# Kernel tuning notes

Hardware: AMD Instinct MI355X
Metric: run time of the kernel (lower is better)

The kernel has to match this reference:

```python
import jax, jax.numpy as jnp
from jax import lax
import numpy as np

THRESHOLD = 0.9
KHALF = 5  # conv_kernel_size; full conv width = 2*KHALF + 1 = 11


def _cif_scan(eouts, alpha_norm, elens, ylens, Lp1):
    """Vectorized-over-batch integrate-and-fire scan over time (lax.scan)."""
    B, T, D = eouts.shape
    bidx = jnp.arange(B)
    dt = eouts.dtype

    def step(carry, xs):
        alpha_accum, state, n_tok, fired = carry
        a_t, e_t, t = xs  # a_t: [B], e_t: [B,D], t: scalar int
        alpha_accum = alpha_accum + a_t
        active = (t <= elens - 1) & (n_tok < ylens)
        fire = active & (alpha_accum >= THRESHOLD)
        ak1 = 1.0 - alpha_accum
        ak2 = a_t - ak1
        # attention-weight column for time t
        aw_col = jnp.zeros((B, Lp1), dt)
        w_old = jnp.where(fire, ak1, jnp.where(active, a_t, jnp.zeros((), dt)))
        aw_col = aw_col.at[bidx, n_tok].add(w_old)
        n_new = n_tok + fire.astype(n_tok.dtype)
        aw_col = aw_col.at[bidx, n_new].add(jnp.where(fire, ak2, jnp.zeros((), dt)))
        # fired output row (set once per token slot)
        fire_val = state + ak1[:, None] * e_t
        cur = fired[bidx, n_tok]
        fired = fired.at[bidx, n_tok].set(jnp.where(fire[:, None], fire_val, cur))
        # integrate / reset state
        state = jnp.where(fire[:, None], ak2[:, None] * e_t,
                          jnp.where(active[:, None], state + a_t[:, None] * e_t, state))
        alpha_accum = jnp.where(fire, ak2, alpha_accum)
        return (alpha_accum, state, n_new, fired), aw_col

    init = (jnp.zeros((B,), dt), jnp.zeros((B, D), dt),
            jnp.zeros((B,), jnp.int32), jnp.zeros((B, Lp1, D), dt))
    xs = (jnp.swapaxes(alpha_norm, 0, 1), jnp.swapaxes(eouts, 0, 1),
          jnp.arange(T))
    (_, _, _, fired), aw_cols = lax.scan(step, init, xs)
    aws = jnp.transpose(aw_cols, (1, 2, 0))[:, None]  # [B,1,Lp1,T]
    return fired, aws


def _forward(eouts, conv_w, conv_b, proj_w, proj_b, elens, ylens, L):
    # Conv1d over time, 'same' padding: [B,T,D] -> [B,T,C]
    conv_feat = lax.conv_general_dilated(
        eouts, conv_w, window_strides=(1,), padding=[(KHALF, KHALF)],
        dimension_numbers=('NWC', 'WIO', 'NWC')) + conv_b
    alpha = jax.nn.sigmoid(conv_feat @ proj_w + proj_b)[:, :, 0]  # [B,T]
    alpha_norm = alpha / jnp.sum(alpha, axis=1, keepdims=True) \
        * ylens[:, None].astype(alpha.dtype)
    fired, aws = _cif_scan(eouts, alpha_norm, elens, ylens, L + 1)
    return fired[:, :L], alpha, aws


def setup_inputs():
    key = jax.random.key(0)
    k1, k2, k3, k4, k5 = jax.random.split(key, 5)
    B, T, D, C = 16, 2048, 512, 512
    eouts = jax.random.normal(k1, (B, T, D), jnp.float32)
    elens = jnp.maximum(jax.random.randint(k2, (B,), 0, T), T // 2).astype(jnp.int32)
    ylens = jnp.maximum(jax.random.randint(k3, (B,), 0, 128), 32).astype(jnp.int32)
    conv_w = jax.random.normal(k4, (2 * KHALF + 1, D, C), jnp.float32) * 0.02
    conv_b = jnp.zeros((C,), jnp.float32)
    proj_w = jax.random.normal(k5, (C, 1), jnp.float32) * 0.05
    proj_b = jnp.zeros((1,), jnp.float32)
    return dict(eouts=eouts, conv_w=conv_w, conv_b=conv_b,
                proj_w=proj_w, proj_b=proj_b, elens=elens, ylens=ylens)


def reference(eouts, conv_w, conv_b, proj_w, proj_b, elens, ylens):
    L = int(jnp.max(ylens))  # max_len = ylens.max(), as in the original
    return _forward(eouts, conv_w, conv_b, proj_w, proj_b, elens, ylens, L)
```

## Files before the change

kernel.cpp:

```cpp
#include <hip/hip_runtime.h>
#include <math.h>

#define KHALF 5
#define MAXF 256

__global__ void k_weff(const float* __restrict__ conv_w, const float* __restrict__ conv_b,
                       const float* __restrict__ proj_w, const float* __restrict__ proj_b,
                       float* __restrict__ w_eff, float* __restrict__ b_eff,
                       int KD, int C) {
    int gid = blockIdx.x * blockDim.x + threadIdx.x;
    int wave = gid >> 6;
    int lane = gid & 63;
    if (wave > KD) return;
    float s = 0.f;
    if (wave < KD) {
        const float* row = conv_w + (size_t)wave * C;
        for (int c = lane * 4; c < C; c += 256) {
            float4 v = *reinterpret_cast<const float4*>(row + c);
            float4 w = *reinterpret_cast<const float4*>(proj_w + c);
            s += v.x * w.x + v.y * w.y + v.z * w.z + v.w * w.w;
        }
    } else {
        for (int c = lane; c < C; c += 64) s += conv_b[c] * proj_w[c];
    }
#pragma unroll
    for (int off = 32; off > 0; off >>= 1) s += __shfl_down(s, off, 64);
    if (lane == 0) {
        if (wave < KD) w_eff[wave] = s;
        else           b_eff[0] = s + proj_b[0];
    }
}

__global__ __launch_bounds__(256) void k_qdot(const float* __restrict__ eouts,
                                              const float* __restrict__ w_eff,
                                              float* __restrict__ q, int BT) {
    __shared__ float tile[64 * 68];
    __shared__ float wls[11 * 68];
    __shared__ float part[64 * 89];
    const int u0 = blockIdx.x * 64;
    const int rp = threadIdx.x & 31;
    const int s8 = threadIdx.x >> 5;
    float acc0[11], acc1[11];
#pragma unroll
    for (int k = 0; k < 11; ++k) { acc0[k] = 0.f; acc1[k] = 0.f; }
    for (int c = 0; c < 8; ++c) {
        __syncthreads();
#pragma unroll
        for (int it = 0; it < 4; ++it) {
            int idx = it * 256 + threadIdx.x;
            int r = idx >> 4, j4 = idx & 15;
            float4 v = *reinterpret_cast<const float4*>(
                eouts + (size_t)(u0 + r) * 512 + c * 64 + j4 * 4);
            *reinterpret_cast<float4*>(&tile[r * 68 + j4 * 4]) = v;
        }
        if (threadIdx.x < 176) {
            int k = threadIdx.x >> 4, sl = threadIdx.x & 15;
            float4 wv = *reinterpret_cast<const float4*>(
                w_eff + k * 512 + c * 64 + sl * 4);
            *reinterpret_cast<float4*>(&wls[k * 68 + sl * 4]) = wv;
        }
        __syncthreads();
#pragma unroll
        for (int j4 = 0; j4 < 2; ++j4) {
            const int dl = s8 * 8 + j4 * 4;
            float4 a0 = *reinterpret_cast<const float4*>(&tile[rp * 68 + dl]);
            float4 a1 = *reinterpret_cast<const float4*>(&tile[(rp + 32) * 68 + dl]);
#pragma unroll
            for (int k = 0; k < 11; ++k) {
                float4 wv = *reinterpret_cast<const float4*>(&wls[k * 68 + dl]);
                acc0[k] += a0.x * wv.x + a0.y * wv.y + a0.z * wv.z + a0.w * wv.w;
                acc1[k] += a1.x * wv.x + a1.y * wv.y + a1.z * wv.z + a1.w * wv.w;
            }
        }
    }
    __syncthreads();
#pragma unroll
    for (int k = 0; k < 11; ++k) {
        part[rp * 89 + s8 * 11 + k] = acc0[k];
        part[(rp + 32) * 89 + s8 * 11 + k] = acc1[k];
    }
    __syncthreads();
    if (threadIdx.x < 64) {
        int r = threadIdx.x;
        const float* p = &part[r * 89];
        float o[12];
#pragma unroll
        for (int k = 0; k < 11; ++k) {
            float s0 = (p[0 * 11 + k] + p[1 * 11 + k]) + (p[2 * 11 + k] + p[3 * 11 + k]);
            float s1 = (p[4 * 11 + k] + p[5 * 11 + k]) + (p[6 * 11 + k] + p[7 * 11 + k]);
            o[k] = s0 + s1;
        }
        o[11] = 0.f;
        float4* dst = reinterpret_cast<float4*>(q + (size_t)(u0 + r) * 12);
        dst[0] = make_float4(o[0], o[1], o[2], o[3]);
        dst[1] = make_float4(o[4], o[5], o[6], o[7]);
        dst[2] = make_float4(o[8], o[9], o[10], o[11]);
    }
}

__global__ __launch_bounds__(256) void k_sigpart(const float* __restrict__ q,
                                                 const float* __restrict__ b_eff,
                                                 float* __restrict__ alpha,
                                                 float* __restrict__ partials,
                                                 int T, int tcb) {
    __shared__ float qs[266 * 12];
    __shared__ float psm[4];
    int bx = blockIdx.x;
    int b = bx / tcb, tc = bx % tcb;
    int t0 = tc * 256;
    const float* qb = q + (size_t)b * T * 12;
    const int base = (t0 - 5) * 12;
    const int lim = T * 12;
    for (int i = threadIdx.x; i < 266 * 12; i += 256) {
        int gi = base + i;
        qs[i] = (gi >= 0 && gi < lim) ? qb[gi] : 0.f;
    }
    __syncthreads();
    int t = t0 + threadIdx.x;
    float sacc = b_eff[0];
#pragma unroll
    for (int k = 0; k < 11; ++k) sacc += qs[(threadIdx.x + k) * 12 + k];
    float al = 1.f / (1.f + expf(-sacc));
    alpha[(size_t)b * T + t] = al;
    float s = al;
    int lane = threadIdx.x & 63;
    int w = threadIdx.x >> 6;
#pragma unroll
    for (int off = 32; off > 0; off >>= 1) s += __shfl_down(s, off, 64);
    if (lane == 0) psm[w] = s;
    __syncthreads();
    if (threadIdx.x == 0) {
        float tot = 0.f;
        for (int i = 0; i < 4; ++i) tot += psm[i];
        partials[bx] = tot;
    }
}

__global__ void k_alpha(const float* __restrict__ eouts,
                        const float* __restrict__ w_eff,
                        const float* __restrict__ b_eff,
                        float* __restrict__ alpha,
                        int B, int T, int D) {
    const int W = 2 * KHALF + 1;
    int gid = blockIdx.x * blockDim.x + threadIdx.x;
    int wave = gid >> 6;
    int lane = gid & 63;
    if (wave >= B * T) return;
    int b = wave / T;
    int t = wave - b * T;
    int WD = W * D;
    int t0 = t - KHALF;
    float s = 0.f;
    if (t0 >= 0 && t0 + W <= T) {
        const float* base = eouts + ((size_t)b * T + t0) * D;
        for (int j = lane * 4; j < WD; j += 256) {
            float4 v = *reinterpret_cast<const float4*>(base + j);
            float4 w = *reinterpret_cast<const float4*>(w_eff + j);
            s += v.x * w.x + v.y * w.y + v.z * w.z + v.w * w.w;
        }
    } else {
        const float* base = eouts + (size_t)b * T * D;
        for (int j = lane; j < WD; j += 64) {
            int tt = t0 + j / D;
            if (tt >= 0 && tt < T) {
                int d = j - (j / D) * D;
                s += base[(size_t)tt * D + d] * w_eff[j];
            }
        }
    }
#pragma unroll
    for (int off = 32; off > 0; off >>= 1) s += __shfl_down(s, off, 64);
    if (lane == 0) {
        float logit = s + b_eff[0];
        alpha[(size_t)b * T + t] = 1.f / (1.f + expf(-logit));
    }
}

__global__ void k_chain(const float* __restrict__ alpha_in,
                        int use_part,
                        const float* __restrict__ partials, int npart,
                        const int* __restrict__ elens,
                        const int* __restrict__ ylens,
                        float* __restrict__ alpha_sum,
                        float* __restrict__ anorm,
                        int* __restrict__ n_fired,
                        int* __restrict__ fire_t,
                        float* __restrict__ fire_a1,
                        float* __restrict__ fire_a2,
                        int T, int Lp1) {
    extern __shared__ float an[];
    __shared__ float sm[16];
    __shared__ float stot;
    int b = blockIdx.x;
    const float* row = alpha_in + (size_t)b * T;
    for (int i = threadIdx.x; i < T; i += blockDim.x) an[i] = row[i];
    __syncthreads();
    if (use_part) {
        if (threadIdx.x == 0) {
            float tot = 0.f;
            for (int i = 0; i < npart; ++i) tot += partials[b * npart + i];
            stot = tot;
            alpha_sum[b] = tot;
        }
    } else {
        float s = 0.f;
        for (int i = threadIdx.x; i < T; i += blockDim.x) s += an[i];
        int lane0 = threadIdx.x & 63;
        int w0 = threadIdx.x >> 6;
#pragma unroll
        for (int off = 32; off > 0; off >>= 1) s += __shfl_down(s, off, 64);
        if (lane0 == 0) sm[w0] = s;
        __syncthreads();
        if (threadIdx.x == 0) {
            float tot = 0.f;
            int nw = blockDim.x >> 6;
            for (int i = 0; i < nw; ++i) tot += sm[i];
            stot = tot;
            alpha_sum[b] = tot;
        }
    }
    __syncthreads();
    float ssum = stot;
    float yl = (float)ylens[b];
    float* __restrict__ anb = anorm + (size_t)b * T;
    for (int i = threadIdx.x; i < T; i += blockDim.x) {
        float v = an[i] / ssum * yl;
        an[i] = v;
        anb[i] = v;
    }
    __syncthreads();
    if (threadIdx.x >= 64) return;
    int lane = threadIdx.x;
    int elen = elens[b];
    if (elen > T) elen = T;
    const int ylen = ylens[b];
    int* __restrict__ ft = fire_t + (size_t)b * Lp1;
    float* __restrict__ fa1 = fire_a1 + (size_t)b * Lp1;
    float* __restrict__ fa2 = fire_a2 + (size_t)b * Lp1;
    float accum = 0.f;
    int n = 0;
    bool done = false;
    for (int t0 = 0; t0 < elen && !done; t0 += 64) {
        int nv = elen - t0;
        if (nv > 64) nv = 64;
        float a = (lane < nv) ? an[t0 + lane] : 0.f;
        float P = a;
#pragma unroll
        for (int off = 1; off < 64; off <<= 1) {
            float tmp = __shfl_up(P, off, 64);
            if (lane >= off) P += tmp;
        }
        unsigned long long validmask = (nv == 64) ? ~0ull : ((1ull << nv) - 1ull);
        float base = accum;
        int start = 0;
        while (true) {
            bool cond = (base + P >= 0.9f);
            unsigned long long bal = __ballot(cond) & validmask;
            if (start > 0) bal &= (~0ull) << start;
            if (bal == 0) break;
            int u = __builtin_ctzll(bal);
            float Pu = __shfl(P, u, 64);
            float au = __shfl(a, u, 64);
            float accum_f = base + Pu;
            float ak1 = 1.f - accum_f;
            float ak2 = au - ak1;
            if (lane == 0) { ft[n] = t0 + u; fa1[n] = ak1; fa2[n] = ak2; }
            ++n;
            if (n >= ylen) { done = true; break; }
            base = ak2 - Pu;
            start = u + 1;
            if (start >= nv) break;
        }
        if (!done) {
            float Plast = __shfl(P, nv - 1, 64);
            accum = base + Plast;
        }
    }
    if (lane == 0) n_fired[b] = n;
}

__global__ void k_awfired(const float* __restrict__ eouts,
                          const float* __restrict__ anorm,
                          const int* __restrict__ elens,
                          const int* __restrict__ ylens,
                          const int* __restrict__ n_fired,
                          const int* __restrict__ fire_t,
                          const float* __restrict__ fire_a1,
                          const float* __restrict__ fire_a2,
                          float* __restrict__ aws,
                          float* __restrict__ fired,
                          int T, int D, int L, int Lp1,
                          int AB, int tcpb, int DB) {
    if ((int)blockIdx.x < AB) {
        __shared__ int fts[MAXF];
        __shared__ float a1s[MAXF];
        __shared__ float a2s[MAXF];
        int b = blockIdx.x / tcpb;
        int tc = blockIdx.x % tcpb;
        int nf = n_fired[b];
        for (int i = threadIdx.x; i < nf; i += blockDim.x) {
            fts[i] = fire_t[(size_t)b * Lp1 + i];
            a1s[i] = fire_a1[(size_t)b * Lp1 + i];
            a2s[i] = fire_a2[(size_t)b * Lp1 + i];
        }
        __syncthreads();
        int t = tc * 256 + threadIdx.x;
        if (t >= T) return;
        int elen = elens[b];
        if (elen > T) elen = T;
        int ylen = ylens[b];
        bool active = (t < elen);
        int rowi = 0;
        bool isfire = false;
        float v1 = 0.f, v2 = 0.f;
        if (active) {
            int lo = 0, hi = nf;
            while (lo < hi) {
                int mid = (lo + hi) >> 1;
                if (fts[mid] < t) lo = mid + 1; else hi = mid;
            }
            rowi = lo;
            isfire = (rowi < nf && fts[rowi] == t);
            if (isfire) { v1 = a1s[rowi]; v2 = a2s[rowi]; }
            else if (rowi < ylen) v1 = anorm[(size_t)b * T + t];
            else active = false;
        }
        float* col = aws + (size_t)b * Lp1 * T + t;
        for (int r = 0; r < Lp1; ++r) {
            float v = 0.f;
            if (active) {
                if (r == rowi) v = v1;
                else if (isfire && r == rowi + 1) v = v2;
            }
            col[(size_t)r * T] = v;
        }
    } else {
        int idx = blockIdx.x - AB;
        int b = idx / (L * DB);
        int rem = idx % (L * DB);
        int n = rem / DB;
        int d = (rem % DB) * 256 + threadIdx.x;
        if (d >= D) return;
        int nf = n_fired[b];
        float* dst = fired + ((size_t)b * L + n) * D + d;
        if (n >= nf) { *dst = 0.f; return; }
        int t0 = (n == 0) ? 0 : fire_t[(size_t)b * Lp1 + n - 1];
        int t1 = fire_t[(size_t)b * Lp1 + n];
        float ak1 = fire_a1[(size_t)b * Lp1 + n];
        float ak2p = (n > 0) ? fire_a2[(size_t)b * Lp1 + n - 1] : 0.f;
        const float* an_g = anorm + (size_t)b * T;
        const float* e = eouts + ((size_t)b * T + t0) * D + d;
        float accv = 0.f;
        for (int t = t0; t <= t1; ++t, e += D) {
            float wgt;
            if (t == t1) wgt = ak1;
            else if (t == t0 && n > 0) wgt = ak2p;
            else wgt = an_g[t];
            accv += wgt * e[0];
        }
        *dst = accv;
    }
}

extern "C" void kernel_launch(void* const* d_in, const int* in_sizes, int n_in,
                              void* d_out, int out_size, void* d_ws, size_t ws_size,
                              hipStream_t stream) {
    const float* eouts  = (const float*)d_in[0];
    const float* conv_w = (const float*)d_in[1];
    const float* conv_b = (const float*)d_in[2];
    const float* proj_w = (const float*)d_in[3];
    const float* proj_b = (const float*)d_in[4];
    const int*   elens  = (const int*)d_in[5];
    const int*   ylens  = (const int*)d_in[6];

    const int B = in_sizes[5];
    const int C = in_sizes[2];
    const int W = 2 * KHALF + 1;
    const int D = in_sizes[1] / (W * C);
    const int T = in_sizes[0] / (B * D);
    const int L = (out_size - 2 * B * T) / (B * (D + T));
    const int Lp1 = L + 1;
    const int BT = B * T;
    const int tcb = (T + 255) / 256;

    float* out   = (float*)d_out;
    float* fired = out;
    float* alpha = out + (size_t)B * L * D;
    float* aws   = alpha + (size_t)B * T;

    char*  ws        = (char*)d_ws;
    float* w_eff     = (float*)ws;
    float* b_eff     = (float*)(ws + (size_t)W * D * 4);
    float* alpha_sum = b_eff + 16;
    int*   n_fired   = (int*)(alpha_sum + B + 16);
    int*   fire_t    = n_fired + B + 16;
    float* fire_a1   = (float*)(fire_t + (size_t)B * Lp1 + 16);
    float* fire_a2   = fire_a1 + (size_t)B * Lp1 + 16;
    float* anorm     = fire_a2 + (size_t)B * Lp1 + 16;
    float* qbuf      = anorm + (size_t)B * T + 16;
    float* partials  = qbuf + (size_t)BT * 12 + 16;
    size_t ws_need   = (size_t)((char*)(partials + (size_t)B * tcb + 16) - ws);

    const int KD = W * D;
    {
        long long threads = (long long)(KD + 1) * 64;
        int blocks = (int)((threads + 255) / 256);
        k_weff<<<blocks, 256, 0, stream>>>(conv_w, conv_b, proj_w, proj_b,
                                           w_eff, b_eff, KD, C);
    }

    const bool fast = (ws_size >= ws_need) && (D == 512) && (C == 512) &&
                      (BT % 64 == 0) && (T % 256 == 0) && (T <= 16384) &&
                      (Lp1 <= MAXF);
    if (fast) {
        k_qdot<<<BT / 64, 256, 0, stream>>>(eouts, w_eff, qbuf, BT);
        k_sigpart<<<B * tcb, 256, 0, stream>>>(qbuf, b_eff, alpha, partials, T, tcb);
    } else {
        long long threads = (long long)BT * 64;
        int blocks = (int)((threads + 255) / 256);
        k_alpha<<<blocks, 256, 0, stream>>>(eouts, w_eff, b_eff, alpha, B, T, D);
    }

    k_chain<<<B, 256, T * sizeof(float), stream>>>(
        alpha, fast ? 1 : 0, partials, tcb,
        elens, ylens, alpha_sum, anorm,
        n_fired, fire_t, fire_a1, fire_a2, T, Lp1);

    {
        int tcpb = (T + 255) / 256;
        int AB = B * tcpb;
        int DB = (D + 255) / 256;
        int FB = B * L * DB;
        k_awfired<<<AB + FB, 256, 0, stream>>>(eouts, anorm,
                                               elens, ylens, n_fired,
                                               fire_t, fire_a1, fire_a2,
                                               aws, fired, T, D, L, Lp1,
                                               AB, tcpb, DB);
    }
}
```

Baseline: 181.7 us.

## Precompute chunk prefix sums in parallel, unroll fired gather, shrink aws tiles

In the chain kernel, all four waves now compute per-64-element prefix sums into shared memory up front, so the serial single-wave fire loop only reads them instead of doing a shuffle scan per chunk. The alpha load is vectorised to float4 and the partial sums are staged through shared memory. The fired-row accumulation loop is unrolled by four with separate accumulators and the branchy weight selection removed. The aws part now gives each block 128 time steps, leaving half of its 256 threads idle. This adds more blocks and changes the float summation order.

```diff
diff --git a/kernel.cpp b/kernel.cpp
--- a/kernel.cpp
+++ b/kernel.cpp
@@ -189,16 +189,27 @@
                         float* __restrict__ fire_a2,
                         int T, int Lp1) {
     extern __shared__ float an[];
+    float* pf = an + T;
     __shared__ float sm[16];
     __shared__ float stot;
     int b = blockIdx.x;
     const float* row = alpha_in + (size_t)b * T;
-    for (int i = threadIdx.x; i < T; i += blockDim.x) an[i] = row[i];
+    if ((T & 1023) == 0) {
+        const float4* r4 = reinterpret_cast<const float4*>(row);
+        float4* a4 = reinterpret_cast<float4*>(an);
+        for (int i = threadIdx.x; i < (T >> 2); i += blockDim.x) a4[i] = r4[i];
+    } else {
+        for (int i = threadIdx.x; i < T; i += blockDim.x) an[i] = row[i];
+    }
     __syncthreads();
     if (use_part) {
+        if (threadIdx.x < npart && threadIdx.x < 16)
+            sm[threadIdx.x] = partials[b * npart + threadIdx.x];
+        __syncthreads();
         if (threadIdx.x == 0) {
             float tot = 0.f;
-            for (int i = 0; i < npart; ++i) tot += partials[b * npart + i];
+            if (npart <= 16) { for (int i = 0; i < npart; ++i) tot += sm[i]; }
+            else { for (int i = 0; i < npart; ++i) tot += partials[b * npart + i]; }
             stot = tot;
             alpha_sum[b] = tot;
         }
@@ -227,6 +238,21 @@
         float v = an[i] / ssum * yl;
         an[i] = v;
         anb[i] = v;
+    }
+    __syncthreads();
+    {
+        int wv = threadIdx.x >> 6, ln = threadIdx.x & 63;
+        int nchunks = (T + 63) >> 6;
+        for (int c = wv; c < nchunks; c += 4) {
+            int t = c * 64 + ln;
+            float P = (t < T) ? an[t] : 0.f;
+#pragma unroll
+            for (int off = 1; off < 64; off <<= 1) {
+                float tmp = __shfl_up(P, off, 64);
+                if (ln >= off) P += tmp;
+            }
+            if (t < T) pf[t] = P;
+        }
     }
     __syncthreads();
     if (threadIdx.x >= 64) return;
@@ -243,13 +269,7 @@
     for (int t0 = 0; t0 < elen && !done; t0 += 64) {
         int nv = elen - t0;
         if (nv > 64) nv = 64;
-        float a = (lane < nv) ? an[t0 + lane] : 0.f;
-        float P = a;
-#pragma unroll
-        for (int off = 1; off < 64; off <<= 1) {
-            float tmp = __shfl_up(P, off, 64);
-            if (lane >= off) P += tmp;
-        }
+        float P = (t0 + lane < T) ? pf[t0 + lane] : 0.f;
         unsigned long long validmask = (nv == 64) ? ~0ull : ((1ull << nv) - 1ull);
         float base = accum;
         int start = 0;
@@ -259,8 +279,8 @@
             if (start > 0) bal &= (~0ull) << start;
             if (bal == 0) break;
             int u = __builtin_ctzll(bal);
-            float Pu = __shfl(P, u, 64);
-            float au = __shfl(a, u, 64);
+            float Pu = pf[t0 + u];
+            float au = an[t0 + u];
             float accum_f = base + Pu;
             float ak1 = 1.f - accum_f;
             float ak2 = au - ak1;
@@ -271,10 +291,7 @@
             start = u + 1;
             if (start >= nv) break;
         }
-        if (!done) {
-            float Plast = __shfl(P, nv - 1, 64);
-            accum = base + Plast;
-        }
+        if (!done) accum = base + pf[t0 + nv - 1];
     }
     if (lane == 0) n_fired[b] = n;
 }
@@ -304,7 +321,8 @@
             a2s[i] = fire_a2[(size_t)b * Lp1 + i];
         }
         __syncthreads();
-        int t = tc * 256 + threadIdx.x;
+        if (threadIdx.x >= 128) return;
+        int t = tc * 128 + threadIdx.x;
         if (t >= T) return;
         int elen = elens[b];
         if (elen > T) elen = T;
@@ -350,13 +368,24 @@
         float ak2p = (n > 0) ? fire_a2[(size_t)b * Lp1 + n - 1] : 0.f;
         const float* an_g = anorm + (size_t)b * T;
         const float* e = eouts + ((size_t)b * T + t0) * D + d;
-        float accv = 0.f;
-        for (int t = t0; t <= t1; ++t, e += D) {
-            float wgt;
-            if (t == t1) wgt = ak1;
-            else if (t == t0 && n > 0) wgt = ak2p;
-            else wgt = an_g[t];
-            accv += wgt * e[0];
+        float accv;
+        if (t1 == t0) {
+            accv = ak1 * e[0];
+        } else {
+            float w0 = (n > 0) ? ak2p : an_g[t0];
+            accv = w0 * e[0];
+            float a0 = 0.f, a1 = 0.f, a2 = 0.f, a3 = 0.f;
+            int t = t0 + 1;
+            const float* ee = e + D;
+            for (; t + 3 < t1; t += 4, ee += 4 * (size_t)D) {
+                a0 += an_g[t]     * ee[0];
+                a1 += an_g[t + 1] * ee[D];
+                a2 += an_g[t + 2] * ee[2 * (size_t)D];
+                a3 += an_g[t + 3] * ee[3 * (size_t)D];
+            }
+            for (; t < t1; ++t, ee += D) a0 += an_g[t] * ee[0];
+            accv += ((a0 + a1) + (a2 + a3));
+            accv += ak1 * ee[0];
         }
         *dst = accv;
     }
@@ -421,13 +450,13 @@
         k_alpha<<<blocks, 256, 0, stream>>>(eouts, w_eff, b_eff, alpha, B, T, D);
     }
 
-    k_chain<<<B, 256, T * sizeof(float), stream>>>(
+    k_chain<<<B, 256, 2 * T * sizeof(float), stream>>>(
         alpha, fast ? 1 : 0, partials, tcb,
         elens, ylens, alpha_sum, anorm,
         n_fired, fire_t, fire_a1, fire_a2, T, Lp1);
 
     {
-        int tcpb = (T + 255) / 256;
+        int tcpb = (T + 127) / 128;
         int AB = B * tcpb;
         int DB = (D + 255) / 256;
         int FB = B * L * DB;
```

Result: faster. 163.6 us (-9.9%).
